# Performance work log

Hardware: AMD Instinct MI355X
Metric: run time of the kernel (lower is better)

The kernel has to match this reference:

```python
import jax, jax.numpy as jnp
import numpy as np

B, S, D, H, G = 64, 1024, 512, 1024, 4096  # G = 4*H


def setup_inputs() -> dict:
    key = jax.random.key(0)
    ks = jax.random.split(key, 9)
    s = lambda fan: 1.0 / np.sqrt(H)  # torch LSTMCell init scale
    return {
        "x": jax.random.normal(ks[0], (B, S, D), dtype=jnp.float32),
        "W_ih0": jax.random.uniform(ks[1], (G, D), jnp.float32, -s(D), s(D)),
        "W_hh0": jax.random.uniform(ks[2], (G, H), jnp.float32, -s(H), s(H)),
        "b_ih0": jax.random.uniform(ks[3], (G,), jnp.float32, -s(H), s(H)),
        "b_hh0": jax.random.uniform(ks[4], (G,), jnp.float32, -s(H), s(H)),
        "W_ih1": jax.random.uniform(ks[5], (G, H), jnp.float32, -s(H), s(H)),
        "W_hh1": jax.random.uniform(ks[6], (G, H), jnp.float32, -s(H), s(H)),
        "b_ih1": jax.random.uniform(ks[7], (G,), jnp.float32, -s(H), s(H)),
        "b_hh1": jax.random.uniform(ks[8], (G,), jnp.float32, -s(H), s(H)),
    }


def _lstm_cell(x, h, c, W_ih, W_hh, b_ih, b_hh):
    # gates ordered i, f, g, o as in torch.nn.LSTMCell
    gates = x @ W_ih.T + b_ih + h @ W_hh.T + b_hh  # [B, 4H]
    i, f, g, o = jnp.split(gates, 4, axis=-1)
    c_new = jax.nn.sigmoid(f) * c + jax.nn.sigmoid(i) * jnp.tanh(g)
    h_new = jax.nn.sigmoid(o) * jnp.tanh(c_new)
    return h_new, c_new


def reference(x, W_ih0, W_hh0, b_ih0, b_hh0, W_ih1, W_hh1, b_ih1, b_hh1):
    batch = x.shape[0]
    zeros = jnp.zeros((batch, H), dtype=x.dtype)

    def step(carry, x_t):
        h0, c0, h1, c1 = carry
        h0, c0 = _lstm_cell(x_t, h0, c0, W_ih0, W_hh0, b_ih0, b_hh0)
        h1, c1 = _lstm_cell(h0, h1, c1, W_ih1, W_hh1, b_ih1, b_hh1)
        return (h0, c0, h1, c1), (h1, c1)

    carry0 = (zeros, zeros, zeros, zeros)
    xs = jnp.swapaxes(x, 0, 1)  # [S, B, D]
    (h0, c0, h1, c1), (hs, cs) = jax.lax.scan(step, carry0, xs)
    out = jnp.swapaxes(hs, 0, 1)    # [B, S, H] top-layer h per step
    c_out = jnp.swapaxes(cs, 0, 1)  # [B, S, H] top-layer c per step
    return (out, c_out, h1, c1)
```

## Files before the change

### kernel.cpp

```cpp
#include <hip/hip_runtime.h>
#include <stdint.h>

#define B_   64
#define S_   1024
#define D_   512
#define H_   1024
#define G_   4096
#define NWG  256

using bf16x8 = __attribute__((ext_vector_type(8))) short;
using f32x16 = __attribute__((ext_vector_type(16))) float;

#define FLAG_OFF  0
#define RING_OFF  4096
#define SLOT_BYTES 131072
#define BSUM_OFF  532480
#define BFRAG_OFF 1048576
#define B0_PER_WG 98304
#define B1_OFF    (BFRAG_OFF + 128*B0_PER_WG)
#define B1_PER_WG 131072

#define COUT_OFF 67108864ll
#define HF_OFF   134217728ll
#define CF_OFF   134283264ll

__device__ __forceinline__ uint16_t f2bf(float f) {
  uint32_t u = __float_as_uint(f);
  u += 0x7FFFu + ((u >> 16) & 1u);
  return (uint16_t)(u >> 16);
}
__device__ __forceinline__ float sigf(float x)  { return 1.0f / (1.0f + __expf(-x)); }
__device__ __forceinline__ float tanhf_(float x){ return 2.0f / (1.0f + __expf(-2.0f * x)) - 1.0f; }

__global__ void prep_misc(const float* __restrict__ bih0, const float* __restrict__ bhh0,
                          const float* __restrict__ bih1, const float* __restrict__ bhh1,
                          char* __restrict__ ws) {
  int tid = blockIdx.x * 256 + threadIdx.x;
  if (tid < 132096) { ((uint32_t*)ws)[tid] = 0u; return; }
  int i = tid - 132096;
  if (i < 8192) {
    int L = i >> 12, g = i & 4095;
    float v = L ? (bih1[g] + bhh1[g]) : (bih0[g] + bhh0[g]);
    ((float*)(ws + BSUM_OFF))[L * 4096 + g] = v;
  }
}

__global__ void prep_w(const float* __restrict__ Wih0, const float* __restrict__ Whh0,
                       const float* __restrict__ Wih1, const float* __restrict__ Whh1,
                       char* __restrict__ ws) {
  int tid = blockIdx.x * 256 + threadIdx.x;
  if (tid >= 7340032) return;
  uint32_t* dst = (uint32_t*)(ws + BFRAG_OFF);
  int layer, wg, ks, lane, jp;
  if (tid < 3145728) { layer = 0; wg = tid / 24576; int rem = tid % 24576; ks = rem >> 8; int r2 = rem & 255; lane = r2 >> 2; jp = r2 & 3; }
  else { int t2 = tid - 3145728; layer = 1; wg = t2 / 32768; int rem = t2 % 32768; ks = rem >> 8; int r2 = rem & 255; lane = r2 >> 2; jp = r2 & 3; }
  int n = lane & 31;
  int row = (n >> 3) * 1024 + wg * 8 + (n & 7);
  int k = ks * 16 + ((lane >> 5) << 3) + jp * 2;
  float w0, w1;
  if (!layer) {
    if (k < 512) { w0 = Wih0[row * 512 + k];          w1 = Wih0[row * 512 + k + 1]; }
    else         { w0 = Whh0[row * 1024 + k - 512];   w1 = Whh0[row * 1024 + k - 511]; }
  } else {
    if (k < 1024){ w0 = Wih1[row * 1024 + k];         w1 = Wih1[row * 1024 + k + 1]; }
    else         { w0 = Whh1[row * 1024 + k - 1024];  w1 = Whh1[row * 1024 + k - 1023]; }
  }
  dst[tid] = (uint32_t)f2bf(w0) | ((uint32_t)f2bf(w1) << 16);
}

__global__ void prep_x(const float* __restrict__ x, float* __restrict__ out) {
  int tid = blockIdx.x * 256 + threadIdx.x;
  if (tid >= 16777216) return;
  int t = tid >> 14;
  int sidx = tid & 16383;
  int jp = sidx & 3;
  int lane = (sidx >> 2) & 63;
  int mtks = sidx >> 8;
  int mt = mtks & 1, ks = mtks >> 1;
  int b = mt * 32 + (lane & 31);
  int k = ks * 16 + ((lane >> 5) << 3) + jp * 2;
  const float* xp = x + ((long)b * S_ + t) * D_ + k;
  uint32_t v = (uint32_t)f2bf(xp[0]) | ((uint32_t)f2bf(xp[1]) << 16);
  ((uint32_t*)(out + COUT_OFF))[(long)(sidx >> 10) * 1048576 + ((long)t << 10) + (sidx & 1023)] = v;
}

__global__ void __launch_bounds__(256) lstm_main(float* __restrict__ out, char* __restrict__ ws) {
  const int tid = threadIdx.x;
  const int lane = tid & 63;
  const int wave = tid >> 6;
  const int wg = blockIdx.x;
  const int layer = wg >> 7;
  const int cw = wg & 127;

  uint32_t* flags = (uint32_t*)(ws + FLAG_OFF);
  const float* bsum = (const float*)(ws + BSUM_OFF) + layer * G_;
  const char* bwg = ws + (layer ? (B1_OFF + (size_t)cw * B1_PER_WG)
                                : (BFRAG_OFF + (size_t)cw * B0_PER_WG));
  float* coutF = out + COUT_OFF;

  __shared__ float red[4][64][33];

  float cst0 = 0.f, cst1 = 0.f;
  const int ksteps = layer ? 128 : 96;
  const int kspw = ksteps >> 2;
  const int ks0 = wave * kspw;

  for (int t = 0; t <= S_; ++t) {
    if (t) {
      __syncthreads();
      if (tid == 0) {
        __threadfence();
        __hip_atomic_store(flags + (size_t)wg * 4, (uint32_t)t,
                           __ATOMIC_RELEASE, __HIP_MEMORY_SCOPE_AGENT);
      }
      while (__hip_atomic_load(flags + (size_t)tid * 4,
                               __ATOMIC_RELAXED, __HIP_MEMORY_SCOPE_AGENT) < (uint32_t)t)
        __builtin_amdgcn_s_sleep(1);
      __syncthreads();
      if (tid == 0) __threadfence();
      __syncthreads();
    }
    const bool active = layer ? (t >= 1) : (t < S_);
    if (active) {
      const char* slotH0 = ws + RING_OFF + (size_t)((t - 1) & 1) * SLOT_BYTES;
      const char* slotH1 = ws + RING_OFF + (size_t)(2 + (t & 1)) * SLOT_BYTES;

      f32x16 acc0 = {}; f32x16 acc1 = {};
#pragma unroll 4
      for (int s = 0; s < kspw; ++s) {
        const int ks = ks0 + s;
        const char *a0p, *a1p;
        if (layer == 0) {
          if (ks < 32) {
            int s0 = ((ks * 2 + 0) * 64 + lane) * 4;
            int s1 = ((ks * 2 + 1) * 64 + lane) * 4;
            a0p = (const char*)(coutF + (((long)(s0 >> 10)) << 20) + ((long)t << 10) + (s0 & 1023));
            a1p = (const char*)(coutF + (((long)(s1 >> 10)) << 20) + ((long)t << 10) + (s1 & 1023));
          } else {
            int k2 = ks - 32;
            a0p = slotH0 + ((k2 * 2 + 0) * 64 + lane) * 16;
            a1p = slotH0 + ((k2 * 2 + 1) * 64 + lane) * 16;
          }
        } else {
          if (ks < 64) {
            a0p = slotH0 + ((ks * 2 + 0) * 64 + lane) * 16;
            a1p = slotH0 + ((ks * 2 + 1) * 64 + lane) * 16;
          } else {
            int k2 = ks - 64;
            a0p = slotH1 + ((k2 * 2 + 0) * 64 + lane) * 16;
            a1p = slotH1 + ((k2 * 2 + 1) * 64 + lane) * 16;
          }
        }
        bf16x8 av0 = *(const bf16x8*)a0p;
        bf16x8 av1 = *(const bf16x8*)a1p;
        bf16x8 bv  = *(const bf16x8*)(bwg + (size_t)ks * 1024 + lane * 16);
        acc0 = __builtin_amdgcn_mfma_f32_32x32x16_bf16(av0, bv, acc0, 0, 0, 0);
        acc1 = __builtin_amdgcn_mfma_f32_32x32x16_bf16(av1, bv, acc1, 0, 0, 0);
      }
      const int col = lane & 31;
      const int rbase = 4 * (lane >> 5);
#pragma unroll
      for (int r = 0; r < 16; ++r) {
        int row = (r & 3) + 8 * (r >> 2) + rbase;
        red[wave][row][col] = acc0[r];
        red[wave][32 + row][col] = acc1[r];
      }
      __syncthreads();

      const int b = lane;
      const int mt = b >> 5;
      char* pub = ws + RING_OFF + (size_t)((layer << 1) + ((layer ? (t - 1) : t) & 1)) * SLOT_BYTES;
#pragma unroll
      for (int r = 0; r < 2; ++r) {
        int cc = wave + 4 * r;
        int hc = cw * 8 + cc;
        float g0 = red[0][b][cc]      + red[1][b][cc]      + red[2][b][cc]      + red[3][b][cc]      + bsum[hc];
        float g1 = red[0][b][8 + cc]  + red[1][b][8 + cc]  + red[2][b][8 + cc]  + red[3][b][8 + cc]  + bsum[1024 + hc];
        float g2 = red[0][b][16 + cc] + red[1][b][16 + cc] + red[2][b][16 + cc] + red[3][b][16 + cc] + bsum[2048 + hc];
        float g3 = red[0][b][24 + cc] + red[1][b][24 + cc] + red[2][b][24 + cc] + red[3][b][24 + cc] + bsum[3072 + hc];
        float cprev = r ? cst1 : cst0;
        float cn = sigf(g1) * cprev + sigf(g0) * tanhf_(g2);
        float hn = sigf(g3) * tanhf_(cn);
        if (r) cst1 = cn; else cst0 = cn;
        int ksh = hc >> 4, rem = hc & 15;
        int laned = (b & 31) + ((rem >> 3) << 5);
        ((uint16_t*)pub)[((ksh * 2 + mt) * 64 + laned) * 8 + (rem & 7)] = f2bf(hn);
        if (layer) {
          long s_ = t - 1;
          long idx = ((long)b << 20) + (s_ << 10) + hc;
          __builtin_nontemporal_store(hn, out + idx);
          __builtin_nontemporal_store(cn, out + COUT_OFF + idx);
          if (s_ == S_ - 1) {
            __builtin_nontemporal_store(hn, out + HF_OFF + ((long)b << 10) + hc);
            __builtin_nontemporal_store(cn, out + CF_OFF + ((long)b << 10) + hc);
          }
        }
      }
    }
  }
}

extern "C" void kernel_launch(void* const* d_in, const int* in_sizes, int n_in,
                              void* d_out, int out_size, void* d_ws, size_t ws_size,
                              hipStream_t stream) {
  const float* x    = (const float*)d_in[0];
  const float* Wih0 = (const float*)d_in[1];
  const float* Whh0 = (const float*)d_in[2];
  const float* bih0 = (const float*)d_in[3];
  const float* bhh0 = (const float*)d_in[4];
  const float* Wih1 = (const float*)d_in[5];
  const float* Whh1 = (const float*)d_in[6];
  const float* bih1 = (const float*)d_in[7];
  const float* bhh1 = (const float*)d_in[8];
  float* out = (float*)d_out;
  char* ws = (char*)d_ws;

  hipLaunchKernelGGL(prep_misc, dim3((140288 + 255) / 256), dim3(256), 0, stream, bih0, bhh0, bih1, bhh1, ws);
  hipLaunchKernelGGL(prep_w,    dim3(7340032 / 256),        dim3(256), 0, stream, Wih0, Whh0, Wih1, Whh1, ws);
  hipLaunchKernelGGL(prep_x,    dim3(16777216 / 256),       dim3(256), 0, stream, x, out);

  void* args[] = { (void*)&out, (void*)&ws };
  hipLaunchCooperativeKernel((void*)lstm_main, dim3(NWG), dim3(256), args, 0, stream);
}
```

Measured before the change: 35.42 ms.

## Keep per-workgroup weights resident in LDS and use a counter-based grid barrier

Each workgroup copies its weight fragments (up to 128KB) into LDS once, so the 1024 timesteps read B from LDS instead of global memory. The wave split changes from four K-quarters each computing both M tiles to two M tiles times two K halves, which halves the cross-wave reduction. The grid barrier moves from every thread polling 256 per-workgroup flags to a single atomic counter plus a generation word. The output stores also drop their nontemporal hint. The large LDS footprint limits each CU to one workgroup, and the single counter concentrates atomics on one address.

```diff
diff --git a/kernel.cpp b/kernel.cpp
--- a/kernel.cpp
+++ b/kernel.cpp
@@ -11,7 +11,8 @@
 using bf16x8 = __attribute__((ext_vector_type(8))) short;
 using f32x16 = __attribute__((ext_vector_type(16))) float;
 
-#define FLAG_OFF  0
+#define CNT_OFF   0
+#define GEN_OFF   128
 #define RING_OFF  4096
 #define SLOT_BYTES 131072
 #define BSUM_OFF  532480
@@ -19,6 +20,9 @@
 #define B0_PER_WG 98304
 #define B1_OFF    (BFRAG_OFF + 128*B0_PER_WG)
 #define B1_PER_WG 131072
+
+#define BLDS_BYTES 131072
+#define SMEM_TOTAL 147968
 
 #define COUT_OFF 67108864ll
 #define HF_OFF   134217728ll
@@ -85,39 +89,51 @@
 }
 
 __global__ void __launch_bounds__(256) lstm_main(float* __restrict__ out, char* __restrict__ ws) {
+  extern __shared__ char smem[];
+  float (*red)[64][33] = (float (*)[64][33])(smem + BLDS_BYTES);
+
   const int tid = threadIdx.x;
   const int lane = tid & 63;
   const int wave = tid >> 6;
   const int wg = blockIdx.x;
   const int layer = wg >> 7;
   const int cw = wg & 127;
-
-  uint32_t* flags = (uint32_t*)(ws + FLAG_OFF);
+  const int mt = wave >> 1;
+  const int kh = wave & 1;
+
+  uint32_t* bar_cnt = (uint32_t*)(ws + CNT_OFF);
+  uint32_t* bar_gen = (uint32_t*)(ws + GEN_OFF);
   const float* bsum = (const float*)(ws + BSUM_OFF) + layer * G_;
   const char* bwg = ws + (layer ? (B1_OFF + (size_t)cw * B1_PER_WG)
                                 : (BFRAG_OFF + (size_t)cw * B0_PER_WG));
   float* coutF = out + COUT_OFF;
 
-  __shared__ float red[4][64][33];
+  const int ksteps = layer ? 128 : 96;
+  const int ksph = ksteps >> 1;
+
+  {
+    const int nchunk = ksteps << 6;
+    for (int i = tid; i < nchunk; i += 256)
+      *(bf16x8*)(smem + (size_t)i * 16) = *(const bf16x8*)(bwg + (size_t)i * 16);
+  }
+  __syncthreads();
 
   float cst0 = 0.f, cst1 = 0.f;
-  const int ksteps = layer ? 128 : 96;
-  const int kspw = ksteps >> 2;
-  const int ks0 = wave * kspw;
 
   for (int t = 0; t <= S_; ++t) {
     if (t) {
       __syncthreads();
       if (tid == 0) {
         __threadfence();
-        __hip_atomic_store(flags + (size_t)wg * 4, (uint32_t)t,
-                           __ATOMIC_RELEASE, __HIP_MEMORY_SCOPE_AGENT);
-      }
-      while (__hip_atomic_load(flags + (size_t)tid * 4,
-                               __ATOMIC_RELAXED, __HIP_MEMORY_SCOPE_AGENT) < (uint32_t)t)
-        __builtin_amdgcn_s_sleep(1);
-      __syncthreads();
-      if (tid == 0) __threadfence();
+        uint32_t prev = __hip_atomic_fetch_add(bar_cnt, 1u, __ATOMIC_RELAXED, __HIP_MEMORY_SCOPE_AGENT);
+        if (prev == (uint32_t)(t * NWG - 1)) {
+          __hip_atomic_store(bar_gen, (uint32_t)t, __ATOMIC_RELEASE, __HIP_MEMORY_SCOPE_AGENT);
+        } else {
+          while (__hip_atomic_load(bar_gen, __ATOMIC_RELAXED, __HIP_MEMORY_SCOPE_AGENT) < (uint32_t)t)
+            __builtin_amdgcn_s_sleep(1);
+        }
+        __threadfence();
+      }
       __syncthreads();
     }
     const bool active = layer ? (t >= 1) : (t < S_);
@@ -125,77 +141,70 @@
       const char* slotH0 = ws + RING_OFF + (size_t)((t - 1) & 1) * SLOT_BYTES;
       const char* slotH1 = ws + RING_OFF + (size_t)(2 + (t & 1)) * SLOT_BYTES;
 
-      f32x16 acc0 = {}; f32x16 acc1 = {};
-#pragma unroll 4
-      for (int s = 0; s < kspw; ++s) {
-        const int ks = ks0 + s;
-        const char *a0p, *a1p;
+      f32x16 acc = {};
+#pragma unroll 8
+      for (int s = 0; s < ksph; ++s) {
+        const int ks = kh * ksph + s;
+        const char* ap;
         if (layer == 0) {
           if (ks < 32) {
-            int s0 = ((ks * 2 + 0) * 64 + lane) * 4;
-            int s1 = ((ks * 2 + 1) * 64 + lane) * 4;
-            a0p = (const char*)(coutF + (((long)(s0 >> 10)) << 20) + ((long)t << 10) + (s0 & 1023));
-            a1p = (const char*)(coutF + (((long)(s1 >> 10)) << 20) + ((long)t << 10) + (s1 & 1023));
+            int si = ((ks * 2 + mt) * 64 + lane) * 4;
+            ap = (const char*)(coutF + (((long)(si >> 10)) << 20) + ((long)t << 10) + (si & 1023));
           } else {
             int k2 = ks - 32;
-            a0p = slotH0 + ((k2 * 2 + 0) * 64 + lane) * 16;
-            a1p = slotH0 + ((k2 * 2 + 1) * 64 + lane) * 16;
+            ap = slotH0 + ((k2 * 2 + mt) * 64 + lane) * 16;
           }
         } else {
           if (ks < 64) {
-            a0p = slotH0 + ((ks * 2 + 0) * 64 + lane) * 16;
-            a1p = slotH0 + ((ks * 2 + 1) * 64 + lane) * 16;
+            ap = slotH0 + ((ks * 2 + mt) * 64 + lane) * 16;
           } else {
             int k2 = ks - 64;
-            a0p = slotH1 + ((k2 * 2 + 0) * 64 + lane) * 16;
-            a1p = slotH1 + ((k2 * 2 + 1) * 64 + lane) * 16;
+            ap = slotH1 + ((k2 * 2 + mt) * 64 + lane) * 16;
           }
         }
-        bf16x8 av0 = *(const bf16x8*)a0p;
-        bf16x8 av1 = *(const bf16x8*)a1p;
-        bf16x8 bv  = *(const bf16x8*)(bwg + (size_t)ks * 1024 + lane * 16);
-        acc0 = __builtin_amdgcn_mfma_f32_32x32x16_bf16(av0, bv, acc0, 0, 0, 0);
-        acc1 = __builtin_amdgcn_mfma_f32_32x32x16_bf16(av1, bv, acc1, 0, 0, 0);
+        bf16x8 av = *(const bf16x8*)ap;
+        bf16x8 bv = *(const bf16x8*)(smem + (size_t)ks * 1024 + (size_t)lane * 16);
+        acc = __builtin_amdgcn_mfma_f32_32x32x16_bf16(av, bv, acc, 0, 0, 0);
       }
       const int col = lane & 31;
       const int rbase = 4 * (lane >> 5);
 #pragma unroll
       for (int r = 0; r < 16; ++r) {
         int row = (r & 3) + 8 * (r >> 2) + rbase;
-        red[wave][row][col] = acc0[r];
-        red[wave][32 + row][col] = acc1[r];
+        red[kh][mt * 32 + row][col] = acc[r];
       }
       __syncthreads();
 
       const int b = lane;
-      const int mt = b >> 5;
+      const int bmt = b >> 5;
       char* pub = ws + RING_OFF + (size_t)((layer << 1) + ((layer ? (t - 1) : t) & 1)) * SLOT_BYTES;
 #pragma unroll
       for (int r = 0; r < 2; ++r) {
         int cc = wave + 4 * r;
         int hc = cw * 8 + cc;
-        float g0 = red[0][b][cc]      + red[1][b][cc]      + red[2][b][cc]      + red[3][b][cc]      + bsum[hc];
-        float g1 = red[0][b][8 + cc]  + red[1][b][8 + cc]  + red[2][b][8 + cc]  + red[3][b][8 + cc]  + bsum[1024 + hc];
-        float g2 = red[0][b][16 + cc] + red[1][b][16 + cc] + red[2][b][16 + cc] + red[3][b][16 + cc] + bsum[2048 + hc];
-        float g3 = red[0][b][24 + cc] + red[1][b][24 + cc] + red[2][b][24 + cc] + red[3][b][24 + cc] + bsum[3072 + hc];
+        float g0 = red[0][b][cc]      + red[1][b][cc]      + bsum[hc];
+        float g1 = red[0][b][8 + cc]  + red[1][b][8 + cc]  + bsum[1024 + hc];
+        float g2 = red[0][b][16 + cc] + red[1][b][16 + cc] + bsum[2048 + hc];
+        float g3 = red[0][b][24 + cc] + red[1][b][24 + cc] + bsum[3072 + hc];
         float cprev = r ? cst1 : cst0;
         float cn = sigf(g1) * cprev + sigf(g0) * tanhf_(g2);
         float hn = sigf(g3) * tanhf_(cn);
         if (r) cst1 = cn; else cst0 = cn;
         int ksh = hc >> 4, rem = hc & 15;
         int laned = (b & 31) + ((rem >> 3) << 5);
-        ((uint16_t*)pub)[((ksh * 2 + mt) * 64 + laned) * 8 + (rem & 7)] = f2bf(hn);
+        ((uint16_t*)pub)[((ksh * 2 + bmt) * 64 + laned) * 8 + (rem & 7)] = f2bf(hn);
         if (layer) {
           long s_ = t - 1;
           long idx = ((long)b << 20) + (s_ << 10) + hc;
-          __builtin_nontemporal_store(hn, out + idx);
-          __builtin_nontemporal_store(cn, out + COUT_OFF + idx);
+          out[idx] = hn;
+          out[COUT_OFF + idx] = cn;
           if (s_ == S_ - 1) {
-            __builtin_nontemporal_store(hn, out + HF_OFF + ((long)b << 10) + hc);
-            __builtin_nontemporal_store(cn, out + CF_OFF + ((long)b << 10) + hc);
+            out[HF_OFF + ((long)b << 10) + hc] = hn;
+            out[CF_OFF + ((long)b << 10) + hc] = cn;
           }
         }
       }
+      __syncthreads();
     }
   }
 }
@@ -215,10 +224,17 @@
   float* out = (float*)d_out;
   char* ws = (char*)d_ws;
 
+  static bool attr_set = false;
+  if (!attr_set) {
+    (void)hipFuncSetAttribute((const void*)lstm_main,
+                              hipFuncAttributeMaxDynamicSharedMemorySize, SMEM_TOTAL);
+    attr_set = true;
+  }
+
   hipLaunchKernelGGL(prep_misc, dim3((140288 + 255) / 256), dim3(256), 0, stream, bih0, bhh0, bih1, bhh1, ws);
   hipLaunchKernelGGL(prep_w,    dim3(7340032 / 256),        dim3(256), 0, stream, Wih0, Whh0, Wih1, Whh1, ws);
   hipLaunchKernelGGL(prep_x,    dim3(16777216 / 256),       dim3(256), 0, stream, x, out);
 
   void* args[] = { (void*)&out, (void*)&ws };
-  hipLaunchCooperativeKernel((void*)lstm_main, dim3(NWG), dim3(256), args, 0, stream);
-}
+  hipLaunchCooperativeKernel((void*)lstm_main, dim3(NWG), dim3(256), args, SMEM_TOTAL, stream);
+}
```

Result: faster. 34.00 ms (-4.0%).
